# Performance work log

Hardware: AMD Instinct MI355X
Metric: run time of the kernel (lower is better)

## Reference

```python
import math
import jax, jax.numpy as jnp
import numpy as np

T, C, NH = 2048, 1024, 16
HD = C // NH


def setup_inputs() -> dict:
    key = jax.random.key(0)
    ks = jax.random.split(key, 5)
    return {
        "x": jax.random.normal(ks[0], (T, C), dtype=jnp.float32),
        "w_attn": jax.random.normal(ks[1], (3 * C, C), dtype=jnp.float32) * (1.0 / math.sqrt(C)),
        "b_attn": jax.random.normal(ks[2], (3 * C,), dtype=jnp.float32) * 0.02,
        "w_proj": jax.random.normal(ks[3], (C, C), dtype=jnp.float32) * (1.0 / math.sqrt(C)),
        "b_proj": jax.random.normal(ks[4], (C,), dtype=jnp.float32) * 0.02,
    }


def reference(x, w_attn, b_attn, w_proj, b_proj):
    t, c = x.shape
    # qkv projection: eqx Linear computes W @ x + b, vmapped over T
    qkv = x @ w_attn.T + b_attn  # (T, 3C)
    q, k, v = jnp.split(qkv, 3, axis=1)  # each (T, C)
    # (T, NH, HD) -> (NH, T, HD)
    q = jnp.swapaxes(q.reshape(t, NH, HD), 0, 1)
    k = jnp.swapaxes(k.reshape(t, NH, HD), 0, 1)
    v = jnp.swapaxes(v.reshape(t, NH, HD), 0, 1)
    att = jnp.einsum('hqd,hkd->hqk', q, k) / math.sqrt(HD)  # (NH, T, T)
    causal = jnp.tril(jnp.ones((t, t), dtype=bool))
    att = jnp.where(causal[None, :, :], att, -jnp.inf)
    att = jax.nn.softmax(att, axis=-1)
    y = jnp.matmul(att, v)  # (NH, T, HD)
    # Faithful to source: swapaxes(1,2) on (NH, T, HD) -> (NH, HD, T), then reshape
    y = jnp.swapaxes(y, 1, 2).reshape(t, c)
    return y @ w_proj.T + b_proj
```

## Files before the change

kernel.cpp:

```cpp
#include <hip/hip_runtime.h>
#include <hip/hip_bf16.h>
#include <stdint.h>

typedef __bf16 bf16;
typedef __bf16 bf16x8 __attribute__((ext_vector_type(8)));
typedef __bf16 bf16x4 __attribute__((ext_vector_type(4)));
typedef float floatx4 __attribute__((ext_vector_type(4)));

#define T_DIM 2048
#define C_DIM 1024
#define NH    16
#define HD    64

__device__ __forceinline__ void gload_lds16(const void* g, void* l) {
    __builtin_amdgcn_global_load_lds(
        (__attribute__((address_space(1))) void*)(g),
        (__attribute__((address_space(3))) void*)(l),
        16, 0, 0);
}

#define MFMA16(a, b, c) __builtin_amdgcn_mfma_f32_16x16x32_bf16(a, b, c, 0, 0, 0)

__global__ __launch_bounds__(256) void cvt_all(
    const float* __restrict__ x, const float* __restrict__ wa,
    const float* __restrict__ wp,
    bf16* __restrict__ xb, bf16* __restrict__ wab, bf16* __restrict__ wpb)
{
    const int i = blockIdx.x * 256 + threadIdx.x;
    const float* src; bf16* dst; int off;
    if (i < 262144)      { src = x;  dst = xb;  off = i; }
    else if (i < 655360) { src = wa; dst = wab; off = i - 262144; }
    else                 { src = wp; dst = wpb; off = i - 655360; }
    const float4 a = ((const float4*)src)[off * 2];
    const float4 b = ((const float4*)src)[off * 2 + 1];
    bf16x8 o;
    o[0] = (bf16)a.x; o[1] = (bf16)a.y; o[2] = (bf16)a.z; o[3] = (bf16)a.w;
    o[4] = (bf16)b.x; o[5] = (bf16)b.y; o[6] = (bf16)b.z; o[7] = (bf16)b.w;
    *(bf16x8*)(dst + (size_t)off * 8) = o;
}

template<int MODE, int TN>
__global__ __launch_bounds__(256) void csa_gemm_bt(
    const bf16* __restrict__ A, const bf16* __restrict__ B,
    const float* __restrict__ bias,
    void* __restrict__ out0v, bf16* __restrict__ out1, bf16* __restrict__ out2)
{
    constexpr int K = 1024;
    constexpr int MT = (TN == 128) ? 4 : 2;
    __shared__ __align__(16) bf16 sA[128 * 32];
    __shared__ __align__(16) bf16 sB[TN * 32];

    const int tid  = threadIdx.x;
    const int lane = tid & 63;
    const int wid  = tid >> 6;
    const int rowbase = (TN == 128) ? (wid & 1) * 64 : wid * 32;
    const int colbase = (TN == 128) ? (wid >> 1) * 64 : 0;
    const int tileM = blockIdx.x * 128;
    const int tileN = blockIdx.y * TN;

    const int r0 = tid >> 2;
    const int c0 = (tid & 3) * 8;
    const long aBase = (long)(tileM + r0) * K + c0;
    const long bBase = (long)(tileN + r0) * K + c0;

    const int fr   = lane & 15;
    const int quad = lane >> 4;
    const int fc   = quad * 8;

    floatx4 acc[MT][4];
#pragma unroll
    for (int i = 0; i < MT; i++)
#pragma unroll
        for (int j = 0; j < 4; j++) acc[i][j] = (floatx4){0.f, 0.f, 0.f, 0.f};

    for (int k0 = 0; k0 < K; k0 += 32) {
        __syncthreads();
        gload_lds16(A + aBase + k0,                 sA + tid * 8);
        gload_lds16(A + aBase + (long)64 * K + k0,  sA + 2048 + tid * 8);
        gload_lds16(B + bBase + k0,                 sB + tid * 8);
        if (TN == 128)
            gload_lds16(B + bBase + (long)64 * K + k0, sB + 2048 + tid * 8);
        __syncthreads();

        bf16x8 af[MT], bfr[4];
#pragma unroll
        for (int mt = 0; mt < MT; mt++)
            af[mt] = *(const bf16x8*)(sA + (rowbase + mt * 16 + fr) * 32 + fc);
#pragma unroll
        for (int nt = 0; nt < 4; nt++)
            bfr[nt] = *(const bf16x8*)(sB + (colbase + nt * 16 + fr) * 32 + fc);
#pragma unroll
        for (int mt = 0; mt < MT; mt++)
#pragma unroll
            for (int nt = 0; nt < 4; nt++)
                acc[mt][nt] = MFMA16(af[mt], bfr[nt], acc[mt][nt]);
    }

#pragma unroll
    for (int mt = 0; mt < MT; mt++) {
#pragma unroll
        for (int nt = 0; nt < 4; nt++) {
            const int gn = tileN + colbase + nt * 16 + fr;
            const float bv = bias[gn];
            const int gmb = tileM + rowbase + mt * 16 + quad * 4;
            if (MODE == 0) {
                const int which = gn >> 10;
                const int w2 = gn & 1023;
                const int hh = w2 >> 6, d = w2 & 63;
                if (which == 2) {
                    bf16x4 pk;
#pragma unroll
                    for (int r = 0; r < 4; r++) pk[r] = (bf16)(acc[mt][nt][r] + bv);
                    *(bf16x4*)(out2 + ((long)(hh * HD + d) << 11) + gmb) = pk;
                } else {
                    bf16* dst = (which == 0) ? (bf16*)out0v : out1;
#pragma unroll
                    for (int r = 0; r < 4; r++)
                        dst[((long)hh * T_DIM + gmb + r) * HD + d] =
                            (bf16)(acc[mt][nt][r] + bv);
                }
            } else {
#pragma unroll
                for (int r = 0; r < 4; r++)
                    ((float*)out0v)[(long)(gmb + r) * C_DIM + gn] =
                        acc[mt][nt][r] + bv;
            }
        }
    }
}

__global__ __launch_bounds__(256) void csa_attn(
    const bf16* __restrict__ Qh, const bf16* __restrict__ Kh,
    const bf16* __restrict__ Vth, bf16* __restrict__ YY)
{
    __shared__ __align__(16) bf16 sK[2][64 * 64];
    __shared__ __align__(16) bf16 sV[2][64 * 64];
    __shared__ __align__(16) bf16 sP[4][16 * 64];

    const int tid  = threadIdx.x;
    const int lane = tid & 63;
    const int wid  = tid >> 6;
    const int fr   = lane & 15;
    const int quad = lane >> 4;
    const int f7   = fr & 7;
    const int h    = blockIdx.y;
    const int qb   = (int)gridDim.x - 1 - (int)blockIdx.x;
    const int q0   = qb * 64;
    const int qg   = q0 + wid * 16 + fr;

    const bf16* qrow = Qh + ((long)h * T_DIM + qg) * HD;
    const bf16x8 qf0 = *(const bf16x8*)(qrow + quad * 8);
    const bf16x8 qf1 = *(const bf16x8*)(qrow + quad * 8 + 32);

    const int rb   = tid >> 3;
    const int cswz = (tid & 7) ^ (rb & 7);

    auto stage = [&](int b, int k0) {
        gload_lds16(Kh + ((long)(h * T_DIM + k0 + rb) << 6) + cswz * 8,
                    &sK[b][0] + tid * 8);
        gload_lds16(Kh + ((long)(h * T_DIM + k0 + rb + 32) << 6) + cswz * 8,
                    &sK[b][0] + 2048 + tid * 8);
        gload_lds16(Vth + ((long)(h * HD + rb) << 11) + k0 + cswz * 8,
                    &sV[b][0] + tid * 8);
        gload_lds16(Vth + ((long)(h * HD + rb + 32) << 11) + k0 + cswz * 8,
                    &sV[b][0] + 2048 + tid * 8);
    };

    stage(0, 0);

    float l_i = 0.f;
    floatx4 o_acc[4];
#pragma unroll
    for (int d4 = 0; d4 < 4; d4++) o_acc[d4] = (floatx4){0.f, 0.f, 0.f, 0.f};

    for (int kt = 0; kt <= qb; ++kt) {
        __syncthreads();
        if (kt < qb) stage((kt + 1) & 1, (kt + 1) * 64);
        const bf16* K_ = &sK[kt & 1][0];
        const bf16* V_ = &sV[kt & 1][0];
        const int k0 = kt * 64;

        float p[4][4];
#pragma unroll
        for (int nt = 0; nt < 4; nt++) {
            const bf16* kr = K_ + (nt * 16 + fr) * 64;
            const bf16x8 ka0 = *(const bf16x8*)(kr + (quad ^ f7) * 8);
            const bf16x8 ka1 = *(const bf16x8*)(kr + ((quad + 4) ^ f7) * 8);
            floatx4 z = (floatx4){0.f, 0.f, 0.f, 0.f};
            z = MFMA16(ka0, qf0, z);
            z = MFMA16(ka1, qf1, z);
            const int kgb = k0 + nt * 16 + quad * 4;
#pragma unroll
            for (int r = 0; r < 4; r++)
                p[nt][r] = (kgb + r <= qg)
                         ? __builtin_amdgcn_exp2f(z[r] * 0.1803368801f)
                         : 0.f;
        }

        float s = 0.f;
#pragma unroll
        for (int nt = 0; nt < 4; nt++)
#pragma unroll
            for (int r = 0; r < 4; r++) s += p[nt][r];
        s += __shfl_xor(s, 16);
        s += __shfl_xor(s, 32);
        l_i += s;

        bf16* pw = &sP[wid][0];
#pragma unroll
        for (int nt = 0; nt < 4; nt++) {
            bf16x4 pk;
#pragma unroll
            for (int r = 0; r < 4; r++) pk[r] = (bf16)p[nt][r];
            *(bf16x4*)(pw + fr * 64 +
                       (((2 * nt + (quad >> 1)) ^ f7) * 8) + (quad & 1) * 4) = pk;
        }
        asm volatile("s_waitcnt lgkmcnt(0)" ::: "memory");
        const bf16x8 pa0 = *(const bf16x8*)(pw + fr * 64 + (quad ^ f7) * 8);
        const bf16x8 pa1 = *(const bf16x8*)(pw + fr * 64 + ((quad + 4) ^ f7) * 8);

#pragma unroll
        for (int d4 = 0; d4 < 4; d4++) {
            const bf16* vr = V_ + (d4 * 16 + fr) * 64;
            const bf16x8 vb0 = *(const bf16x8*)(vr + (quad ^ f7) * 8);
            const bf16x8 vb1 = *(const bf16x8*)(vr + ((quad + 4) ^ f7) * 8);
            o_acc[d4] = MFMA16(pa0, vb0, o_acc[d4]);
            o_acc[d4] = MFMA16(pa1, vb1, o_acc[d4]);
        }
    }

    const float inv_self = 1.f / l_i;
    float inv[4];
#pragma unroll
    for (int r = 0; r < 4; r++) inv[r] = __shfl(inv_self, quad * 4 + r);

#pragma unroll
    for (int r = 0; r < 4; r++) {
        const int q = q0 + wid * 16 + quad * 4 + r;
        const int rq = q >> 10, cq = q & 1023;
#pragma unroll
        for (int d4 = 0; d4 < 4; d4++) {
            const int d = d4 * 16 + fr;
            YY[(long)(h * 128 + 2 * d + rq) * 1024 + cq] =
                (bf16)(o_acc[d4][r] * inv[r]);
        }
    }
}

extern "C" void kernel_launch(void* const* d_in, const int* in_sizes, int n_in,
                              void* d_out, int out_size, void* d_ws, size_t ws_size,
                              hipStream_t stream) {
    (void)in_sizes; (void)n_in; (void)out_size; (void)ws_size;
    const float* x      = (const float*)d_in[0];
    const float* w_attn = (const float*)d_in[1];
    const float* b_attn = (const float*)d_in[2];
    const float* w_proj = (const float*)d_in[3];
    const float* b_proj = (const float*)d_in[4];

    bf16* xb  = (bf16*)d_ws;
    bf16* wab = xb  + (size_t)T_DIM * C_DIM;
    bf16* wpb = wab + (size_t)3 * C_DIM * C_DIM;
    bf16* Q   = wpb + (size_t)C_DIM * C_DIM;
    bf16* Kp  = Q   + (size_t)NH * T_DIM * HD;
    bf16* Vt  = Kp  + (size_t)NH * T_DIM * HD;
    bf16* YY  = Vt  + (size_t)NH * T_DIM * HD;

    cvt_all<<<3072, 256, 0, stream>>>(x, w_attn, w_proj, xb, wab, wpb);

    csa_gemm_bt<0, 128><<<dim3(16, 24), 256, 0, stream>>>(xb, wab, b_attn, Q, Kp, Vt);
    csa_attn<<<dim3(32, NH), 256, 0, stream>>>(Q, Kp, Vt, YY);
    csa_gemm_bt<1, 64><<<dim3(16, 16), 256, 0, stream>>>(YY, wpb, b_proj, d_out, nullptr, nullptr);
}
```

Before: 163.6 us.

## Split causal attention along the key dimension with a separate combine kernel

Attention work is split into chunks of up to 8 key tiles per block (grid z=4), so long query tiles no longer run as one serial block. Single-chunk tiles write the normalized output directly. Multi-chunk tiles write fp32 partial outputs and row sums to workspace, and a new combine kernel sums them and normalizes. This targets load imbalance and low occupancy (512 blocks of very uneven length), at the cost of an extra launch and extra global memory traffic for the partials. The causal mask is now evaluated only on the diagonal tile. Summing unnormalized exp values without a running max matches the old kernel's scheme.

```diff
diff --git a/kernel.cpp b/kernel.cpp
--- a/kernel.cpp
+++ b/kernel.cpp
@@ -129,13 +129,22 @@
     }
 }
 
-__global__ __launch_bounds__(256) void csa_attn(
+__global__ __launch_bounds__(256) void csa_attn_chunk(
     const bf16* __restrict__ Qh, const bf16* __restrict__ Kh,
-    const bf16* __restrict__ Vth, bf16* __restrict__ YY)
+    const bf16* __restrict__ Vth, float* __restrict__ Opart,
+    float* __restrict__ lpart, bf16* __restrict__ YY)
 {
     __shared__ __align__(16) bf16 sK[2][64 * 64];
     __shared__ __align__(16) bf16 sV[2][64 * 64];
     __shared__ __align__(16) bf16 sP[4][16 * 64];
+
+    const int qt = blockIdx.x;
+    const int h  = blockIdx.y;
+    const int c  = blockIdx.z;
+    const int nk = qt + 1;
+    const int kt0 = c * 8;
+    if (kt0 >= nk) return;
+    const int ktend = (kt0 + 8 < nk) ? kt0 + 8 : nk;
 
     const int tid  = threadIdx.x;
     const int lane = tid & 63;
@@ -143,9 +152,7 @@
     const int fr   = lane & 15;
     const int quad = lane >> 4;
     const int f7   = fr & 7;
-    const int h    = blockIdx.y;
-    const int qb   = (int)gridDim.x - 1 - (int)blockIdx.x;
-    const int q0   = qb * 64;
+    const int q0   = qt * 64;
     const int qg   = q0 + wid * 16 + fr;
 
     const bf16* qrow = Qh + ((long)h * T_DIM + qg) * HD;
@@ -166,19 +173,21 @@
                     &sV[b][0] + 2048 + tid * 8);
     };
 
-    stage(0, 0);
+    stage(0, kt0 * 64);
 
     float l_i = 0.f;
     floatx4 o_acc[4];
 #pragma unroll
     for (int d4 = 0; d4 < 4; d4++) o_acc[d4] = (floatx4){0.f, 0.f, 0.f, 0.f};
 
-    for (int kt = 0; kt <= qb; ++kt) {
+    for (int kt = kt0; kt < ktend; ++kt) {
+        const int it = kt - kt0;
         __syncthreads();
-        if (kt < qb) stage((kt + 1) & 1, (kt + 1) * 64);
-        const bf16* K_ = &sK[kt & 1][0];
-        const bf16* V_ = &sV[kt & 1][0];
+        if (kt + 1 < ktend) stage((it + 1) & 1, (kt + 1) * 64);
+        const bf16* K_ = &sK[it & 1][0];
+        const bf16* V_ = &sV[it & 1][0];
         const int k0 = kt * 64;
+        const bool diag = (kt == qt);
 
         float p[4][4];
 #pragma unroll
@@ -191,10 +200,10 @@
             z = MFMA16(ka1, qf1, z);
             const int kgb = k0 + nt * 16 + quad * 4;
 #pragma unroll
-            for (int r = 0; r < 4; r++)
-                p[nt][r] = (kgb + r <= qg)
-                         ? __builtin_amdgcn_exp2f(z[r] * 0.1803368801f)
-                         : 0.f;
+            for (int r = 0; r < 4; r++) {
+                const float e = __builtin_amdgcn_exp2f(z[r] * 0.1803368801f);
+                p[nt][r] = (!diag || (kgb + r <= qg)) ? e : 0.f;
+            }
         }
 
         float s = 0.f;
@@ -229,20 +238,70 @@
         }
     }
 
-    const float inv_self = 1.f / l_i;
-    float inv[4];
-#pragma unroll
-    for (int r = 0; r < 4; r++) inv[r] = __shfl(inv_self, quad * 4 + r);
-
-#pragma unroll
-    for (int r = 0; r < 4; r++) {
-        const int q = q0 + wid * 16 + quad * 4 + r;
-        const int rq = q >> 10, cq = q & 1023;
-#pragma unroll
-        for (int d4 = 0; d4 < 4; d4++) {
-            const int d = d4 * 16 + fr;
-            YY[(long)(h * 128 + 2 * d + rq) * 1024 + cq] =
-                (bf16)(o_acc[d4][r] * inv[r]);
+    if (kt0 == 0 && ktend == nk) {
+        const float inv_self = 1.f / l_i;
+        float inv[4];
+#pragma unroll
+        for (int r = 0; r < 4; r++) inv[r] = __shfl(inv_self, quad * 4 + r);
+#pragma unroll
+        for (int r = 0; r < 4; r++) {
+            const int q = q0 + wid * 16 + quad * 4 + r;
+            const int rq = q >> 10, cq = q & 1023;
+#pragma unroll
+            for (int d4 = 0; d4 < 4; d4++) {
+                const int d = d4 * 16 + fr;
+                YY[(long)(h * 128 + 2 * d + rq) * 1024 + cq] =
+                    (bf16)(o_acc[d4][r] * inv[r]);
+            }
+        }
+    } else {
+        const long obase = ((long)((h * 32 + qt) * 4 + c)) * 4096;
+#pragma unroll
+        for (int d4 = 0; d4 < 4; d4++)
+#pragma unroll
+            for (int r = 0; r < 4; r++)
+                Opart[obase + (wid * 16 + quad * 4 + r) * 64 + d4 * 16 + fr] =
+                    o_acc[d4][r];
+        if (quad == 0)
+            lpart[((h * 32 + qt) * 4 + c) * 64 + wid * 16 + fr] = l_i;
+    }
+}
+
+__global__ __launch_bounds__(256) void csa_combine(
+    const float* __restrict__ Opart, const float* __restrict__ lpart,
+    bf16* __restrict__ YY)
+{
+    const int qt = blockIdx.x + 8;
+    const int h  = blockIdx.y;
+    const int nc = (qt >> 3) + 1;
+    const int t  = threadIdx.x;
+    const int q  = t >> 2;
+    const int d0 = (t & 3) * 16;
+
+    const long obase = ((long)((h * 32 + qt) * 4)) * 4096 + q * 64 + d0;
+    const int  lbase = (h * 32 + qt) * 4 * 64 + q;
+
+    float4 acc[4] = {};
+    float lq = 0.f;
+    for (int c = 0; c < nc; c++) {
+        const float4* src = (const float4*)(Opart + obase + (long)c * 4096);
+#pragma unroll
+        for (int j = 0; j < 4; j++) {
+            const float4 v = src[j];
+            acc[j].x += v.x; acc[j].y += v.y; acc[j].z += v.z; acc[j].w += v.w;
+        }
+        lq += lpart[lbase + c * 64];
+    }
+    const float inv = 1.f / lq;
+    const int qglob = qt * 64 + q;
+    const int rq = qglob >> 10, cq = qglob & 1023;
+#pragma unroll
+    for (int j = 0; j < 4; j++) {
+        const float vv[4] = {acc[j].x, acc[j].y, acc[j].z, acc[j].w};
+#pragma unroll
+        for (int k = 0; k < 4; k++) {
+            const int d = d0 + j * 4 + k;
+            YY[(long)(h * 128 + 2 * d + rq) * 1024 + cq] = (bf16)(vv[k] * inv);
         }
     }
 }
@@ -264,10 +323,13 @@
     bf16* Kp  = Q   + (size_t)NH * T_DIM * HD;
     bf16* Vt  = Kp  + (size_t)NH * T_DIM * HD;
     bf16* YY  = Vt  + (size_t)NH * T_DIM * HD;
+    float* Opart = (float*)(YY + (size_t)T_DIM * C_DIM);
+    float* lpart = Opart + (size_t)16 * 32 * 4 * 4096;
 
     cvt_all<<<3072, 256, 0, stream>>>(x, w_attn, w_proj, xb, wab, wpb);
 
     csa_gemm_bt<0, 128><<<dim3(16, 24), 256, 0, stream>>>(xb, wab, b_attn, Q, Kp, Vt);
-    csa_attn<<<dim3(32, NH), 256, 0, stream>>>(Q, Kp, Vt, YY);
+    csa_attn_chunk<<<dim3(32, NH, 4), 256, 0, stream>>>(Q, Kp, Vt, Opart, lpart, YY);
+    csa_combine<<<dim3(24, NH), 256, 0, stream>>>(Opart, lpart, YY);
     csa_gemm_bt<1, 64><<<dim3(16, 16), 256, 0, stream>>>(YY, wpb, b_proj, d_out, nullptr, nullptr);
 }
```

Result: faster. 157.0 us (-4.0%).
